# Kernel tuning notes

Hardware: AMD Instinct MI355X
Metric: run time of the kernel (lower is better)

Reference implementation:

```python
import jax, jax.numpy as jnp
import numpy as np

EMBED = 1024
HEADS = 16
HEAD_DIM = EMBED // HEADS


def setup_inputs() -> dict:
    key = jax.random.key(0)
    ks = jax.random.split(key, 9)
    s = 1.0 / np.sqrt(EMBED)
    return {
        "embeddings": jax.random.normal(ks[0], (4, 2048, EMBED), dtype=jnp.float32),
        "wq": jax.random.uniform(ks[1], (EMBED, EMBED), jnp.float32, -s, s),
        "bq": jax.random.uniform(ks[2], (EMBED,), jnp.float32, -s, s),
        "wk": jax.random.uniform(ks[3], (EMBED, EMBED), jnp.float32, -s, s),
        "bk": jax.random.uniform(ks[4], (EMBED,), jnp.float32, -s, s),
        "wv": jax.random.uniform(ks[5], (EMBED, EMBED), jnp.float32, -s, s),
        "bv": jax.random.uniform(ks[6], (EMBED,), jnp.float32, -s, s),
        "wo": jax.random.uniform(ks[7], (EMBED, EMBED), jnp.float32, -s, s),
        "bo": jax.random.uniform(ks[8], (EMBED,), jnp.float32, -s, s),
    }


def reference(embeddings, wq, bq, wk, bk, wv, bv, wo, bo):
    b, s, _ = embeddings.shape
    # Projections: x @ W^T + b (torch nn.Linear convention)
    q = (embeddings @ wq.T + bq).reshape(b, s, HEADS, HEAD_DIM)
    k = (embeddings @ wk.T + bk).reshape(b, s, HEADS, HEAD_DIM)
    v = (embeddings @ wv.T + bv).reshape(b, s, HEADS, HEAD_DIM)
    scale = 1.0 / np.sqrt(HEAD_DIM).astype(np.float32)
    # scores: [b, h, s, s]
    scores = jnp.einsum("bqhd,bkhd->bhqk", q, k) * scale
    probs = jax.nn.softmax(scores, axis=-1)
    attn = jnp.einsum("bhqk,bkhd->bqhd", probs, v).reshape(b, s, EMBED)
    return attn @ wo.T + bo
```

## Files before the change

### kernel.cpp

```cpp
#include <hip/hip_runtime.h>
#include <hip/hip_bf16.h>
#include <math.h>

using bf16x8 = __attribute__((ext_vector_type(8))) short;
using f32x4  = __attribute__((ext_vector_type(4))) float;
using f32x16 = __attribute__((ext_vector_type(16))) float;
using i32x4  = __attribute__((ext_vector_type(4))) int;
using i32x2  = __attribute__((ext_vector_type(2))) int;

#define MFMA_BF16(a, b, c) __builtin_amdgcn_mfma_f32_16x16x32_bf16((a), (b), (c), 0, 0, 0)
#define MFMA32(a, b, c)    __builtin_amdgcn_mfma_f32_32x32x16_bf16((a), (b), (c), 0, 0, 0)

__device__ __forceinline__ float bf2f(short s) {
    union { unsigned u; float f; } v;
    v.u = ((unsigned)(unsigned short)s) << 16;
    return v.f;
}
__device__ __forceinline__ short f2bf(float f) {
    union { float f; unsigned u; } v; v.f = f;
    unsigned r = v.u + 0x7FFF + ((v.u >> 16) & 1);
    return (short)(r >> 16);
}
__device__ __forceinline__ int cvtpk_bf16(float lo, float hi) {
    int r;
    asm("v_cvt_pk_bf16_f32 %0, %1, %2" : "=v"(r) : "v"(lo), "v"(hi));
    return r;
}
__device__ __forceinline__ void permswap(int &a, int &b) {
#if __has_builtin(__builtin_amdgcn_permlane32_swap)
    typedef unsigned u32x2v __attribute__((ext_vector_type(2)));
    u32x2v r = __builtin_amdgcn_permlane32_swap((unsigned)a, (unsigned)b, false, false);
    a = (int)r[0]; b = (int)r[1];
#else
    asm volatile("v_permlane32_swap_b32 %0, %1" : "+v"(a), "+v"(b));
#endif
}
__device__ __forceinline__ float fexp2(float x) {
#if __has_builtin(__builtin_amdgcn_exp2f)
    return __builtin_amdgcn_exp2f(x);
#else
    return exp2f(x);
#endif
}

__device__ __forceinline__ void gload_lds16(const void* g, void* l) {
    __builtin_amdgcn_global_load_lds(
        (const __attribute__((address_space(1))) void*)g,
        (__attribute__((address_space(3))) void*)l, 16, 0, 0);
}

__global__ void detect_dtype(const unsigned short* __restrict__ emb, int* flag) {
    __shared__ int tot;
    if (threadIdx.x == 0) tot = 0;
    __syncthreads();
    int c = 0;
    for (int i = 0; i < 64; i++) {
        unsigned short v = emb[2 * (threadIdx.x * 64 + i)];
        unsigned e = (v >> 7) & 0xFF;
        if (v == 0 || v == 0x8000u || (e >= 97 && e <= 137)) c++;
    }
    atomicAdd(&tot, c);
    __syncthreads();
    if (threadIdx.x == 0) *flag = (tot > 8192) ? 1 : 0;
}

__global__ void convert8(const void* __restrict__ src, short* __restrict__ dst,
                         int n8, const int* __restrict__ flag) {
    int i = blockIdx.x * 256 + threadIdx.x;
    if (i >= n8) return;
    if (*flag) {
        ((bf16x8*)dst)[i] = ((const bf16x8*)src)[i];
    } else {
        const float* f = (const float*)src + (size_t)i * 8;
        bf16x8 o;
#pragma unroll
        for (int j = 0; j < 8; j++) o[j] = f2bf(f[j]);
        ((bf16x8*)dst)[i] = o;
    }
}

__global__ void convert_all(
    const void* __restrict__ w0, const void* __restrict__ w1,
    const void* __restrict__ w2, const void* __restrict__ w3,
    const void* __restrict__ b0, const void* __restrict__ b1,
    const void* __restrict__ b2, const void* __restrict__ b3,
    short* dw0, short* dw1, short* dw2, short* dw3,
    short* db0, short* db1, short* db2, short* db3,
    const int* __restrict__ flag)
{
    int i = blockIdx.x * 256 + threadIdx.x;
    const void* src; short* dst; int idx;
    if (i < 524288) {
        int w = i >> 17; idx = i & 131071;
        src = (w == 0) ? w0 : (w == 1) ? w1 : (w == 2) ? w2 : w3;
        dst = (w == 0) ? dw0 : (w == 1) ? dw1 : (w == 2) ? dw2 : dw3;
    } else {
        int j = i - 524288; int b = j >> 7; idx = j & 127;
        src = (b == 0) ? b0 : (b == 1) ? b1 : (b == 2) ? b2 : b3;
        dst = (b == 0) ? db0 : (b == 1) ? db1 : (b == 2) ? db2 : db3;
    }
    if (*flag) {
        ((bf16x8*)dst)[idx] = ((const bf16x8*)src)[idx];
    } else {
        const float* f = (const float*)src + (size_t)idx * 8;
        bf16x8 o;
#pragma unroll
        for (int j = 0; j < 8; j++) o[j] = f2bf(f[j]);
        ((bf16x8*)dst)[idx] = o;
    }
}

__global__ __launch_bounds__(256) void gemm128(
    const short* __restrict__ A,
    const short* __restrict__ B0, const short* __restrict__ B1,
    const short* __restrict__ B2,
    const short* __restrict__ bias0, const short* __restrict__ bias1,
    const short* __restrict__ bias2,
    void* __restrict__ C0, void* __restrict__ C1, void* __restrict__ C2,
    float s0, float s1, float s2,
    int mode0, int mode1, int mode2,
    const int* __restrict__ flag)
{
    constexpr int M = 8192, N = 1024, Kd = 1024, BK = 32;
    __shared__ __align__(16) short As[3][128 * BK];
    __shared__ __align__(16) short Bs[3][128 * BK];

    const int z = blockIdx.z;
    const short* B    = (z == 0) ? B0    : (z == 1) ? B1    : B2;
    const short* bias = (z == 0) ? bias0 : (z == 1) ? bias1 : bias2;
    void*  C     = (z == 0) ? C0 : (z == 1) ? C1 : C2;
    float  scale = (z == 0) ? s0 : (z == 1) ? s1 : s2;
    int    mode  = (z == 0) ? mode0 : (z == 1) ? mode1 : mode2;

    const int tid  = threadIdx.x;
    const int lane = tid & 63;
    const int wave = tid >> 6;
    const int l31  = lane & 31;
    const int hi   = lane >> 5;

    const int bid = blockIdx.x;
    const int swz = ((bid & 7) << 6) | (bid >> 3);
    const int m0 = (swz >> 3) * 128;
    const int n0 = (swz & 7) * 128;
    const int wm = (wave >> 1) * 64;
    const int wn = (wave & 1) * 64;

    const int srow = lane >> 2;
    const int scol = ((lane & 3) ^ ((lane >> 3) & 3)) * 8;
    const int xr = (l31 >> 1) & 3;

    int fl = 1;
    if (mode == 2) fl = *flag;

    f32x16 acc[2][2];
#pragma unroll
    for (int i = 0; i < 2; i++)
#pragma unroll
        for (int j = 0; j < 2; j++)
#pragma unroll
            for (int r = 0; r < 16; r++) acc[i][j][r] = 0.f;

    auto stage = [&](int bufi, int k) {
#pragma unroll
        for (int t = 0; t < 2; t++) {
            const int r = wave * 32 + t * 16;
            gload_lds16(A + (size_t)(m0 + r + srow) * Kd + k + scol,
                        &As[bufi][r * BK]);
            gload_lds16(B + (size_t)(n0 + r + srow) * Kd + k + scol,
                        &Bs[bufi][r * BK]);
        }
    };

    stage(0, 0);
    stage(1, BK);
    int cur = 0, pre = 2;
    for (int k0 = 0; k0 < Kd; k0 += BK) {
        stage(pre, (k0 + 2 * BK) & (Kd - 1));
        asm volatile("s_waitcnt vmcnt(8)" ::: "memory");
        __builtin_amdgcn_s_barrier();
        __builtin_amdgcn_sched_barrier(0);

        bf16x8 a[2][2], b[2][2];
#pragma unroll
        for (int i = 0; i < 2; i++)
#pragma unroll
            for (int s = 0; s < 2; s++) {
                a[i][s] = *(const bf16x8*)
                    (&As[cur][(wm + i * 32 + l31) * BK + (((s << 1) | hi) ^ xr) * 8]);
                b[i][s] = *(const bf16x8*)
                    (&Bs[cur][(wn + i * 32 + l31) * BK + (((s << 1) | hi) ^ xr) * 8]);
            }
#pragma unroll
        for (int s = 0; s < 2; s++)
#pragma unroll
            for (int i = 0; i < 2; i++)
#pragma unroll
                for (int j = 0; j < 2; j++)
                    acc[i][j] = MFMA32(a[i][s], b[j][s], acc[i][j]);

        asm volatile("s_waitcnt lgkmcnt(0)" ::: "memory");
        __builtin_amdgcn_sched_barrier(0);
        __builtin_amdgcn_s_barrier();
        cur = (cur == 2) ? 0 : cur + 1;
        pre = (pre == 2) ? 0 : pre + 1;
    }

    if (mode == 1) {
#pragma unroll
        for (int j = 0; j < 2; j++) {
            const int col = n0 + wn + j * 32 + l31;
            const float bv = bf2f(bias[col]);
#pragma unroll
            for (int i = 0; i < 2; i++) {
#pragma unroll
                for (int g = 0; g < 4; g++) {
                    const int row = m0 + wm + i * 32 + g * 8 + 4 * hi;
                    const float v0 = (acc[i][j][g * 4 + 0] + bv) * scale;
                    const float v1 = (acc[i][j][g * 4 + 1] + bv) * scale;
                    const float v2 = (acc[i][j][g * 4 + 2] + bv) * scale;
                    const float v3 = (acc[i][j][g * 4 + 3] + bv) * scale;
                    i32x2 dd;
                    dd[0] = cvtpk_bf16(v0, v1);
                    dd[1] = cvtpk_bf16(v2, v3);
                    *(i32x2*)((short*)C + (size_t)col * M + row) = dd;
                }
            }
        }
    } else {
#pragma unroll
        for (int j = 0; j < 2; j++) {
            const int col = n0 + wn + j * 32 + l31;
            const float bv = bf2f(bias[col]);
#pragma unroll
            for (int i = 0; i < 2; i++) {
#pragma unroll
                for (int r = 0; r < 16; r++) {
                    const int row = m0 + wm + i * 32 + (r & 3) + 8 * (r >> 2) + 4 * hi;
                    const float v = (acc[i][j][r] + bv) * scale;
                    if (mode == 0) ((short*)C)[(size_t)row * N + col] = f2bf(v);
                    else {
                        if (fl) ((short*)C)[(size_t)row * N + col] = f2bf(v);
                        else    ((float*)C)[(size_t)row * N + col] = v;
                    }
                }
            }
        }
    }
}

__global__ __launch_bounds__(256) void attn_kernel(
    const short* Q, const short* __restrict__ K,
    const short* __restrict__ Vt, short* Aout)
{
    __shared__ __align__(16) short lds[2][2][64][64];

    const int tid  = threadIdx.x;
    const int lane = tid & 63;
    const int wave = tid >> 6;
    const int l31  = lane & 31;
    const int hi   = lane >> 5;
    const int xr   = (l31 & 7) ^ ((l31 >> 3) & 3);

    const int qt = blockIdx.x;
    const int bh = blockIdx.y;
    const int b  = bh >> 4, h = bh & 15;
    const int q0 = b * 2048 + qt * 128 + wave * 32;
    const int c0 = h * 64;

    const int sr  = lane >> 3;
    const int scb = (lane & 7) ^ sr;
    const int sarr = wave >> 1;

    const short* Kb = K  + (size_t)(b * 2048) * 1024 + c0;
    const short* Vb = Vt + (size_t)c0 * 8192 + b * 2048;

    bf16x8 qf[4];
#pragma unroll
    for (int slot = 0; slot < 4; slot++)
        qf[slot] = *(const bf16x8*)(Q + (size_t)(q0 + l31) * 1024 + c0 + slot * 16 + hi * 8);

    auto stage = [&](int bufi, int kt) {
#pragma unroll
        for (int t = 0; t < 4; t++) {
            const int r0 = ((wave & 1) * 4 + t) * 8;
            const int sc = (scb ^ t) * 8;
            short* dst = &lds[bufi][sarr][r0][0];
            if (sarr == 0)
                gload_lds16(Kb + (size_t)(kt + r0 + sr) * 1024 + sc, dst);
            else
                gload_lds16(Vb + (size_t)(r0 + sr) * 8192 + kt + sc, dst);
        }
    };

    bf16x8 onesf;
#pragma unroll
    for (int j = 0; j < 8; j++) onesf[j] = (short)0x3F80;

    f32x16 o[2], l_acc;
#pragma unroll
    for (int r = 0; r < 16; r++) { o[0][r] = 0.f; o[1][r] = 0.f; l_acc[r] = 0.f; }

    stage(0, 0);
    for (int kt = 0; kt < 2048; kt += 64) {
        const int cur = (kt >> 6) & 1;
        stage(cur ^ 1, (kt + 64) & 2047);
        asm volatile("s_waitcnt vmcnt(4)" ::: "memory");
        __builtin_amdgcn_s_barrier();
        __builtin_amdgcn_sched_barrier(0);

        f32x16 st[2];
#pragma unroll
        for (int blk = 0; blk < 2; blk++) {
#pragma unroll
            for (int r = 0; r < 16; r++) st[blk][r] = 0.f;
#pragma unroll
            for (int slot = 0; slot < 4; slot++) {
                bf16x8 kf = *(const bf16x8*)
                    &lds[cur][0][blk * 32 + l31][(((slot << 1) | hi) ^ xr) * 8];
                st[blk] = MFMA32(kf, qf[slot], st[blk]);
            }
        }

#pragma unroll
        for (int blk = 0; blk < 2; blk++)
#pragma unroll
            for (int r = 0; r < 16; r++)
                st[blk][r] = fexp2(st[blk][r]);

#pragma unroll
        for (int ks = 0; ks < 4; ks++) {
            const int blk = ks >> 1;
            const int rb  = (ks & 1) * 8;
            int A0 = cvtpk_bf16(st[blk][rb + 0], st[blk][rb + 1]);
            int A1 = cvtpk_bf16(st[blk][rb + 2], st[blk][rb + 3]);
            int B0 = cvtpk_bf16(st[blk][rb + 4], st[blk][rb + 5]);
            int B1 = cvtpk_bf16(st[blk][rb + 6], st[blk][rb + 7]);
            permswap(A0, B0);
            permswap(A1, B1);
            i32x4 paw; paw[0] = A0; paw[1] = A1; paw[2] = B0; paw[3] = B1;
            const bf16x8 pf = *(const bf16x8*)&paw;
            l_acc = MFMA32(pf, onesf, l_acc);
#pragma unroll
            for (int dblk = 0; dblk < 2; dblk++) {
                bf16x8 vf = *(const bf16x8*)
                    &lds[cur][1][dblk * 32 + l31][(((ks << 1) | hi) ^ xr) * 8];
                o[dblk] = MFMA32(pf, vf, o[dblk]);
            }
        }

        asm volatile("s_waitcnt lgkmcnt(0)" ::: "memory");
        __builtin_amdgcn_sched_barrier(0);
        __builtin_amdgcn_s_barrier();
    }

#pragma unroll
    for (int r = 0; r < 16; r++) {
        const int qrow = (r & 3) + 8 * (r >> 2) + 4 * hi;
        const float inv = 1.f / l_acc[r];
#pragma unroll
        for (int dblk = 0; dblk < 2; dblk++)
            Aout[(size_t)(q0 + qrow) * 1024 + c0 + dblk * 32 + l31] =
                f2bf(o[dblk][r] * inv);
    }
}

extern "C" void kernel_launch(void* const* d_in, const int* in_sizes, int n_in,
                              void* d_out, int out_size, void* d_ws, size_t ws_size,
                              hipStream_t stream)
{
    const size_t MB = (size_t)1024 * 1024;
    char* ws = (char*)d_ws;

    int*   flagp = (int*)ws;
    short* embC  = (short*)(ws + 1 * MB);
    short* wC[4] = { (short*)(ws + 17 * MB), (short*)(ws + 19 * MB),
                     (short*)(ws + 21 * MB), (short*)(ws + 23 * MB) };
    short* bC[4] = { (short*)(ws + 25 * MB), (short*)(ws + 25 * MB + 4096),
                     (short*)(ws + 25 * MB + 8192), (short*)(ws + 25 * MB + 12288) };

    short *Qb, *Kb, *Vt, *Ab;
    if (ws_size >= 90 * MB) {
        Qb = (short*)(ws + 26 * MB);
        Kb = (short*)(ws + 42 * MB);
        Vt = (short*)(ws + 58 * MB);
        Ab = (short*)(ws + 74 * MB);
    } else {
        Qb = (short*)(ws + 26 * MB);
        Kb = (short*)d_out;
        Vt = (short*)(ws + 42 * MB);
        Ab = Qb;
    }

    detect_dtype<<<1, 256, 0, stream>>>((const unsigned short*)d_in[0], flagp);

    convert8<<<4096, 256, 0, stream>>>(d_in[0], embC, 1048576, flagp);
    convert_all<<<2050, 256, 0, stream>>>(
        d_in[1], d_in[3], d_in[5], d_in[7],
        d_in[2], d_in[4], d_in[6], d_in[8],
        wC[0], wC[1], wC[2], wC[3],
        bC[0], bC[1], bC[2], bC[3], flagp);

    dim3 blk(256);
    gemm128<<<dim3(512, 1, 3), blk, 0, stream>>>(
        embC, wC[0], wC[1], wC[2], bC[0], bC[1], bC[2],
        Qb, Kb, Vt, 0.18033688011112042f, 1.0f, 1.0f, 0, 0, 1, nullptr);

    attn_kernel<<<dim3(16, 64), blk, 0, stream>>>(Qb, Kb, Vt, Ab);

    gemm128<<<dim3(512, 1, 1), blk, 0, stream>>>(
        Ab, wC[3], nullptr, nullptr, bC[3], nullptr, nullptr,
        d_out, nullptr, nullptr, 1.0f, 0.f, 0.f, 2, 0, 0, flagp);
}
```

Measured before the change: 321.8 us.

## Enlarge GEMM tile to 256x128 with 512 threads and BK=64 double buffering

Replaces the 128x128 projection GEMM, which used 256 threads and BK=32 with a triple buffer, by a 256x128 tile using 512 threads (8 waves) and BK=64 with a double buffer. The LDS layout gets a new XOR swizzle and the grid is halved. The aim is more reuse of B per block, fewer barriers per K step and less per-iteration overhead. The cost is half as many blocks, which may leave CUs idle on the single output-projection launch, plus a shallower prefetch pipeline.

```diff
diff --git a/kernel.cpp b/kernel.cpp
--- a/kernel.cpp
+++ b/kernel.cpp
@@ -8,8 +8,7 @@
 using i32x4  = __attribute__((ext_vector_type(4))) int;
 using i32x2  = __attribute__((ext_vector_type(2))) int;
 
-#define MFMA_BF16(a, b, c) __builtin_amdgcn_mfma_f32_16x16x32_bf16((a), (b), (c), 0, 0, 0)
-#define MFMA32(a, b, c)    __builtin_amdgcn_mfma_f32_32x32x16_bf16((a), (b), (c), 0, 0, 0)
+#define MFMA32(a, b, c) __builtin_amdgcn_mfma_f32_32x32x16_bf16((a), (b), (c), 0, 0, 0)
 
 __device__ __forceinline__ float bf2f(short s) {
     union { unsigned u; float f; } v;
@@ -110,7 +109,7 @@
     }
 }
 
-__global__ __launch_bounds__(256) void gemm128(
+__global__ __launch_bounds__(512) void gemm256(
     const short* __restrict__ A,
     const short* __restrict__ B0, const short* __restrict__ B1,
     const short* __restrict__ B2,
@@ -121,9 +120,9 @@
     int mode0, int mode1, int mode2,
     const int* __restrict__ flag)
 {
-    constexpr int M = 8192, N = 1024, Kd = 1024, BK = 32;
-    __shared__ __align__(16) short As[3][128 * BK];
-    __shared__ __align__(16) short Bs[3][128 * BK];
+    constexpr int M = 8192, N = 1024, Kd = 1024, BK = 64;
+    __shared__ __align__(16) short Al[2][256][BK];
+    __shared__ __align__(16) short Bl[2][128][BK];
 
     const int z = blockIdx.z;
     const short* B    = (z == 0) ? B0    : (z == 1) ? B1    : B2;
@@ -137,17 +136,17 @@
     const int wave = tid >> 6;
     const int l31  = lane & 31;
     const int hi   = lane >> 5;
+    const int xr   = (l31 & 7) ^ ((l31 >> 3) & 3);
 
     const int bid = blockIdx.x;
-    const int swz = ((bid & 7) << 6) | (bid >> 3);
-    const int m0 = (swz >> 3) * 128;
+    const int swz = ((bid & 7) << 5) | (bid >> 3);
+    const int m0 = (swz >> 3) * 256;
     const int n0 = (swz & 7) * 128;
     const int wm = (wave >> 1) * 64;
     const int wn = (wave & 1) * 64;
 
-    const int srow = lane >> 2;
-    const int scol = ((lane & 3) ^ ((lane >> 3) & 3)) * 8;
-    const int xr = (l31 >> 1) & 3;
+    const int sr  = lane >> 3;
+    const int scb = (lane & 7) ^ sr;
 
     int fl = 1;
     if (mode == 2) fl = *flag;
@@ -162,47 +161,44 @@
 
     auto stage = [&](int bufi, int k) {
 #pragma unroll
+        for (int t = 0; t < 4; t++) {
+            const int r0 = wave * 32 + t * 8;
+            gload_lds16(A + (size_t)(m0 + r0 + sr) * Kd + k + ((scb ^ t) & 7) * 8,
+                        &Al[bufi][r0][0]);
+        }
+#pragma unroll
         for (int t = 0; t < 2; t++) {
-            const int r = wave * 32 + t * 16;
-            gload_lds16(A + (size_t)(m0 + r + srow) * Kd + k + scol,
-                        &As[bufi][r * BK]);
-            gload_lds16(B + (size_t)(n0 + r + srow) * Kd + k + scol,
-                        &Bs[bufi][r * BK]);
+            const int r0 = wave * 16 + t * 8;
+            const int tb = (wave * 2 + t) & 3;
+            gload_lds16(B + (size_t)(n0 + r0 + sr) * Kd + k + ((scb ^ tb) & 7) * 8,
+                        &Bl[bufi][r0][0]);
         }
     };
 
     stage(0, 0);
-    stage(1, BK);
-    int cur = 0, pre = 2;
     for (int k0 = 0; k0 < Kd; k0 += BK) {
-        stage(pre, (k0 + 2 * BK) & (Kd - 1));
-        asm volatile("s_waitcnt vmcnt(8)" ::: "memory");
+        const int cur = (k0 >> 6) & 1;
+        stage(cur ^ 1, (k0 + BK) & (Kd - 1));
+        asm volatile("s_waitcnt vmcnt(6)" ::: "memory");
         __builtin_amdgcn_s_barrier();
         __builtin_amdgcn_sched_barrier(0);
 
-        bf16x8 a[2][2], b[2][2];
-#pragma unroll
-        for (int i = 0; i < 2; i++)
-#pragma unroll
-            for (int s = 0; s < 2; s++) {
-                a[i][s] = *(const bf16x8*)
-                    (&As[cur][(wm + i * 32 + l31) * BK + (((s << 1) | hi) ^ xr) * 8]);
-                b[i][s] = *(const bf16x8*)
-                    (&Bs[cur][(wn + i * 32 + l31) * BK + (((s << 1) | hi) ^ xr) * 8]);
-            }
-#pragma unroll
-        for (int s = 0; s < 2; s++)
-#pragma unroll
-            for (int i = 0; i < 2; i++)
-#pragma unroll
-                for (int j = 0; j < 2; j++)
-                    acc[i][j] = MFMA32(a[i][s], b[j][s], acc[i][j]);
+#pragma unroll
+        for (int ks = 0; ks < 4; ks++) {
+            const int rc = (((ks << 1) | hi) ^ xr) * 8;
+            bf16x8 a0 = *(const bf16x8*)(&Al[cur][wm + l31][rc]);
+            bf16x8 a1 = *(const bf16x8*)(&Al[cur][wm + 32 + l31][rc]);
+            bf16x8 b0 = *(const bf16x8*)(&Bl[cur][wn + l31][rc]);
+            bf16x8 b1 = *(const bf16x8*)(&Bl[cur][wn + 32 + l31][rc]);
+            acc[0][0] = MFMA32(a0, b0, acc[0][0]);
+            acc[0][1] = MFMA32(a0, b1, acc[0][1]);
+            acc[1][0] = MFMA32(a1, b0, acc[1][0]);
+            acc[1][1] = MFMA32(a1, b1, acc[1][1]);
+        }
 
         asm volatile("s_waitcnt lgkmcnt(0)" ::: "memory");
         __builtin_amdgcn_sched_barrier(0);
         __builtin_amdgcn_s_barrier();
-        cur = (cur == 2) ? 0 : cur + 1;
-        pre = (pre == 2) ? 0 : pre + 1;
     }
 
     if (mode == 1) {
@@ -400,14 +396,14 @@
         wC[0], wC[1], wC[2], wC[3],
         bC[0], bC[1], bC[2], bC[3], flagp);
 
-    dim3 blk(256);
-    gemm128<<<dim3(512, 1, 3), blk, 0, stream>>>(
+    dim3 blk(512);
+    gemm256<<<dim3(256, 1, 3), blk, 0, stream>>>(
         embC, wC[0], wC[1], wC[2], bC[0], bC[1], bC[2],
         Qb, Kb, Vt, 0.18033688011112042f, 1.0f, 1.0f, 0, 0, 1, nullptr);
 
-    attn_kernel<<<dim3(16, 64), blk, 0, stream>>>(Qb, Kb, Vt, Ab);
-
-    gemm128<<<dim3(512, 1, 1), blk, 0, stream>>>(
+    attn_kernel<<<dim3(16, 64), dim3(256), 0, stream>>>(Qb, Kb, Vt, Ab);
+
+    gemm256<<<dim3(256, 1, 1), blk, 0, stream>>>(
         Ab, wC[3], nullptr, nullptr, bC[3], nullptr, nullptr,
         d_out, nullptr, nullptr, 1.0f, 0.f, 0.f, 2, 0, 0, flagp);
 }
```

After: 300.0 us. 6.8% less time.
